# Optimization experiments

Hardware: AMD Instinct MI355X
Metric: run time of the kernel (lower is better)

Reference implementation:

```python
import jax, jax.numpy as jnp
import numpy as np

N_NODES = 50000
N_EDGES = 800000
IN_FEATS = 64
K = 4
OUT_FEATS = 256


def setup_inputs() -> dict:
    key = jax.random.key(0)
    k1, k2, k3, k4, k5 = jax.random.split(key, 5)
    signal = jax.random.normal(k1, (N_NODES, IN_FEATS), dtype=jnp.float32)
    src = jax.random.randint(k2, (N_EDGES,), 0, N_NODES, dtype=jnp.int32)
    dst = jax.random.randint(k3, (N_EDGES,), 0, N_NODES, dtype=jnp.int32)
    lambda_max = jnp.array([2.0], dtype=jnp.float32)  # normalized Laplacian bound
    W = jax.random.normal(k4, (IN_FEATS * K, OUT_FEATS), dtype=jnp.float32) * (1.0 / np.sqrt(IN_FEATS * K))
    b = jax.random.normal(k5, (OUT_FEATS,), dtype=jnp.float32) * 0.01
    return {"signal": signal, "src": src, "dst": dst, "lambda_max": lambda_max, "W": W, "b": b}


def reference(signal, src, dst, lambda_max, W, b):
    n = signal.shape[0]
    # in-degrees, clamped to >= 1, then D^{-1/2}
    deg = jax.ops.segment_sum(jnp.ones_like(dst, dtype=signal.dtype), dst, num_segments=n)
    d_sqrt = jnp.power(jnp.clip(deg, 1.0), -0.5)[:, None]  # [N,1]

    def unn_laplacian(x):
        # D^{-1/2} A D^{-1/2} x via gather-from-src, scatter-sum-to-dst
        h = (x * d_sqrt)[src]                                   # [E,f]
        agg = jax.ops.segment_sum(h, dst, num_segments=n)       # [N,f]
        return agg * d_sqrt

    X0 = signal
    Xs = [X0]
    if K > 1:
        re_norm = 2.0 / lambda_max  # broadcasts over nodes ([1] -> [N,f])
        X1 = -re_norm * unn_laplacian(X0) + X0 * (re_norm - 1.0)
        Xs.append(X1)
        for _ in range(2, K):
            Xi = -2.0 * re_norm * unn_laplacian(X1) + X1 * 2.0 * (re_norm - 1.0) - X0
            Xs.append(Xi)
            X1, X0 = Xi, X1
    Xt = jnp.concatenate(Xs, axis=1)  # [N, f*K]
    return jax.nn.relu(Xt @ W + b)
```

## Files before the change

kernel.cpp:

```cpp
#include <hip/hip_runtime.h>

#define NN 50000
#define NE 800000
#define F  64
#define FK 256
#define OUTF 256
#define CAP 48
#define NT 3128

#define NPART 8
#define PART_NODES 6250
#define FILL_CHUNKS 256
#define CHUNK_E 3125

typedef __attribute__((ext_vector_type(8))) short s16x8;
typedef __attribute__((ext_vector_type(4))) float f32x4;

static __device__ __forceinline__ unsigned short f2bf(float f) {
    unsigned u = __float_as_uint(f);
    u += 0x7fffu + ((u >> 16) & 1u);
    return (unsigned short)(u >> 16);
}
static __device__ __forceinline__ float bf2f(int h) {
    return __uint_as_float(((unsigned)(h & 0xffff)) << 16);
}

__global__ __launch_bounds__(256) void fill_kernel(const int* __restrict__ src,
                                                   const int* __restrict__ dst,
                                                   int* __restrict__ cnt,
                                                   int* __restrict__ csr) {
    int part  = blockIdx.x & (NPART - 1);
    int chunk = blockIdx.x >> 3;
    int lo = part * PART_NODES;
    int e0 = chunk * CHUNK_E;
    int e1 = e0 + CHUNK_E;
    for (int e = e0 + threadIdx.x; e < e1; e += 256) {
        int d = dst[e];
        int s = src[e];
        if ((unsigned)(d - lo) < (unsigned)PART_NODES) {
            int k = atomicAdd(&cnt[d], 1);
            if (k < CAP) csr[d * CAP + k] = s;
        }
    }
}

__global__ void dsqrt_kernel(const int* __restrict__ cnt, float* __restrict__ dsq) {
    int n = blockIdx.x * blockDim.x + threadIdx.x;
    if (n < NN) dsq[n] = rsqrtf(fmaxf((float)cnt[n], 1.0f));
}


__global__ void copy0_kernel(const float* __restrict__ sig,
                             unsigned short* __restrict__ XrowH,
                             unsigned short* __restrict__ XrowL,
                             unsigned short* __restrict__ XfH) {
    int i = blockIdx.x * blockDim.x + threadIdx.x;
    if (i >= NN * 16) return;
    int n = i >> 4, fq = i & 15;
    float4 v = *(const float4*)&sig[n * F + fq * 4];
    unsigned short h0 = f2bf(v.x), h1 = f2bf(v.y), h2 = f2bf(v.z), h3 = f2bf(v.w);
    unsigned short l0 = f2bf(v.x - bf2f(h0)), l1 = f2bf(v.y - bf2f(h1));
    unsigned short l2 = f2bf(v.z - bf2f(h2)), l3 = f2bf(v.w - bf2f(h3));
    *(ushort4*)&XrowH[(size_t)n * 192 + fq * 4] = make_ushort4(h0, h1, h2, h3);
    *(ushort4*)&XrowL[(size_t)n * 192 + fq * 4] = make_ushort4(l0, l1, l2, l3);
    int t = n >> 4, m = n & 15;
    int k0 = fq >> 3, qq = (fq >> 1) & 3, half = fq & 1;
    size_t base = ((size_t)((t * 8 + k0) * 64 + qq * 16 + m)) * 8 + half * 4;
    *(ushort4*)&XfH[base] = make_ushort4(h0, h1, h2, h3);
}

__global__ void convw_kernel(const float* __restrict__ W,
                             unsigned short* __restrict__ WfH,
                             unsigned short* __restrict__ WfL) {
    int id = blockIdx.x * blockDim.x + threadIdx.x;
    if (id >= 8192) return;
    int lane = id & 63, k0 = (id >> 6) & 7, ct = id >> 9;
    int n = lane & 15, q = lane >> 4;
    s16x8 h, l;
    #pragma unroll
    for (int j = 0; j < 8; ++j) {
        float x = W[(k0 * 32 + q * 8 + j) * OUTF + ct * 16 + n];
        unsigned short hh = f2bf(x);
        h[j] = (short)hh;
        l[j] = (short)f2bf(x - bf2f(hh));
    }
    ((s16x8*)WfH)[id] = h;
    ((s16x8*)WfL)[id] = l;
}

__global__ __launch_bounds__(256) void lap_kernel(const int* __restrict__ cnt,
                                                  const int* __restrict__ csr,
                                                  const float* __restrict__ dsq,
                                                  const float* __restrict__ lm,
                                                  unsigned short* __restrict__ XrowH,
                                                  unsigned short* __restrict__ XrowL,
                                                  unsigned short* __restrict__ XfH, int p) {
    int wid  = (blockIdx.x * blockDim.x + threadIdx.x) >> 6;
    int lane = threadIdx.x & 63;
    int q  = lane >> 4;
    int fq = lane & 15;
    if (wid >= NN) return;
    int n  = wid;
    int dg = min(cnt[n], CAP);
    int cin = p - 1;
    int foff = fq << 2;

    float ax = 0.f, ay = 0.f, az = 0.f, aw = 0.f;
    for (int k = q; k < dg; k += 16) {
        int s0 = csr[n * CAP + k];
        int s1 = (k + 4  < dg) ? csr[n * CAP + k + 4]  : s0;
        int s2 = (k + 8  < dg) ? csr[n * CAP + k + 8]  : s0;
        int s3 = (k + 12 < dg) ? csr[n * CAP + k + 12] : s0;
        float d0 = dsq[s0];
        float d1 = (k + 4  < dg) ? dsq[s1] : 0.f;
        float d2 = (k + 8  < dg) ? dsq[s2] : 0.f;
        float d3 = (k + 12 < dg) ? dsq[s3] : 0.f;
        ushort4 h0 = *(const ushort4*)&XrowH[((size_t)s0 * 3 + cin) * 64 + foff];
        ushort4 h1 = *(const ushort4*)&XrowH[((size_t)s1 * 3 + cin) * 64 + foff];
        ushort4 h2 = *(const ushort4*)&XrowH[((size_t)s2 * 3 + cin) * 64 + foff];
        ushort4 h3 = *(const ushort4*)&XrowH[((size_t)s3 * 3 + cin) * 64 + foff];
        ax += bf2f(h0.x) * d0 + bf2f(h1.x) * d1 + bf2f(h2.x) * d2 + bf2f(h3.x) * d3;
        ay += bf2f(h0.y) * d0 + bf2f(h1.y) * d1 + bf2f(h2.y) * d2 + bf2f(h3.y) * d3;
        az += bf2f(h0.z) * d0 + bf2f(h1.z) * d1 + bf2f(h2.z) * d2 + bf2f(h3.z) * d3;
        aw += bf2f(h0.w) * d0 + bf2f(h1.w) * d1 + bf2f(h2.w) * d2 + bf2f(h3.w) * d3;
    }
    ax += __shfl_xor(ax, 16); ax += __shfl_xor(ax, 32);
    ay += __shfl_xor(ay, 16); ay += __shfl_xor(ay, 32);
    az += __shfl_xor(az, 16); az += __shfl_xor(az, 32);
    aw += __shfl_xor(aw, 16); aw += __shfl_xor(aw, 32);

    float rn = 2.0f / lm[0];
    float dn = dsq[n];
    ushort4 xh = *(const ushort4*)&XrowH[((size_t)n * 3 + cin) * 64 + foff];
    ushort4 xl = *(const ushort4*)&XrowL[((size_t)n * 3 + cin) * 64 + foff];
    float x1x = bf2f(xh.x) + bf2f(xl.x);
    float x1y = bf2f(xh.y) + bf2f(xl.y);
    float x1z = bf2f(xh.z) + bf2f(xl.z);
    float x1w = bf2f(xh.w) + bf2f(xl.w);
    float rx, ry, rz, rw;
    if (p == 1) {
        float c1 = rn - 1.0f;
        rx = -rn * dn * ax + x1x * c1;
        ry = -rn * dn * ay + x1y * c1;
        rz = -rn * dn * az + x1z * c1;
        rw = -rn * dn * aw + x1w * c1;
    } else {
        ushort4 zh = *(const ushort4*)&XrowH[((size_t)n * 3 + (p - 2)) * 64 + foff];
        ushort4 zl = *(const ushort4*)&XrowL[((size_t)n * 3 + (p - 2)) * 64 + foff];
        float c1 = 2.0f * (rn - 1.0f);
        rx = -2.0f * rn * dn * ax + x1x * c1 - (bf2f(zh.x) + bf2f(zl.x));
        ry = -2.0f * rn * dn * ay + x1y * c1 - (bf2f(zh.y) + bf2f(zl.y));
        rz = -2.0f * rn * dn * az + x1z * c1 - (bf2f(zh.z) + bf2f(zl.z));
        rw = -2.0f * rn * dn * aw + x1w * c1 - (bf2f(zh.w) + bf2f(zl.w));
    }
    unsigned short h0 = f2bf(rx), h1 = f2bf(ry), h2 = f2bf(rz), h3 = f2bf(rw);

    if (q == 0 && p < 3) {
        *(ushort4*)&XrowH[((size_t)n * 3 + p) * 64 + foff] = make_ushort4(h0, h1, h2, h3);
    } else if (q == 2 && p < 3) {
        unsigned short l0 = f2bf(rx - bf2f(h0)), l1 = f2bf(ry - bf2f(h1));
        unsigned short l2 = f2bf(rz - bf2f(h2)), l3 = f2bf(rw - bf2f(h3));
        *(ushort4*)&XrowL[((size_t)n * 3 + p) * 64 + foff] = make_ushort4(l0, l1, l2, l3);
    } else if (q == 1) {
        int t = n >> 4, m = n & 15;
        int k0 = p * 2 + (fq >> 3), qq = (fq >> 1) & 3, half = fq & 1;
        size_t fbase = ((size_t)((t * 8 + k0) * 64 + qq * 16 + m)) * 8 + half * 4;
        *(ushort4*)&XfH[fbase] = make_ushort4(h0, h1, h2, h3);
    }
}

__global__ __launch_bounds__(512, 2) void gemm_kernel(const unsigned short* __restrict__ XfH,
                                                      const unsigned short* __restrict__ WfH,
                                                      const unsigned short* __restrict__ WfL,
                                                      const float* __restrict__ b,
                                                      float* __restrict__ out) {
    int lane = threadIdx.x & 63;
    int w    = threadIdx.x >> 6;
    int rh = w & 1, cg = w >> 1;
    int m = lane & 15, q = lane >> 4;
    int bt0 = blockIdx.x * 8;
    const s16x8* AH = (const s16x8*)XfH;
    const s16x8* BH = (const s16x8*)WfH;
    const s16x8* BL = (const s16x8*)WfL;

    f32x4 acc[4][4];
    #pragma unroll
    for (int rt = 0; rt < 4; ++rt)
        #pragma unroll
        for (int c = 0; c < 4; ++c) acc[rt][c] = (f32x4){0.f, 0.f, 0.f, 0.f};

    #pragma unroll
    for (int k0 = 0; k0 < 8; ++k0) {
        s16x8 a[4];
        #pragma unroll
        for (int rt = 0; rt < 4; ++rt)
            a[rt] = AH[((bt0 + rh * 4 + rt) * 8 + k0) * 64 + lane];
        #pragma unroll
        for (int c = 0; c < 4; ++c) {
            int ct = cg * 4 + c;
            s16x8 bh = BH[(ct * 8 + k0) * 64 + lane];
            s16x8 bl = BL[(ct * 8 + k0) * 64 + lane];
            #pragma unroll
            for (int rt = 0; rt < 4; ++rt) {
                acc[rt][c] = __builtin_amdgcn_mfma_f32_16x16x32_bf16(a[rt], bh, acc[rt][c], 0, 0, 0);
                acc[rt][c] = __builtin_amdgcn_mfma_f32_16x16x32_bf16(a[rt], bl, acc[rt][c], 0, 0, 0);
            }
        }
    }

    #pragma unroll
    for (int rt = 0; rt < 4; ++rt) {
        int rbase = (bt0 + rh * 4 + rt) * 16 + q * 4;
        #pragma unroll
        for (int c = 0; c < 4; ++c) {
            int col = (cg * 4 + c) * 16 + m;
            float bv = b[col];
            #pragma unroll
            for (int i = 0; i < 4; ++i) {
                int r = rbase + i;
                if (r < NN) out[r * OUTF + col] = fmaxf(acc[rt][c][i] + bv, 0.0f);
            }
        }
    }
}

extern "C" void kernel_launch(void* const* d_in, const int* in_sizes, int n_in,
                              void* d_out, int out_size, void* d_ws, size_t ws_size,
                              hipStream_t stream) {
    const float* signal     = (const float*)d_in[0];
    const int*   src        = (const int*)  d_in[1];
    const int*   dst        = (const int*)  d_in[2];
    const float* lambda_max = (const float*)d_in[3];
    const float* W          = (const float*)d_in[4];
    const float* b          = (const float*)d_in[5];
    float* out = (float*)d_out;

    int*   cnt = (int*)d_ws;
    int*   csr = cnt + NN;
    float* dsq = (float*)(csr + NN * CAP);
    unsigned short* XrowH = (unsigned short*)(dsq + NN);
    unsigned short* XrowL = XrowH + (size_t)NN * 192;
    unsigned short* XfH   = XrowL + (size_t)NN * 192;
    unsigned short* WfH   = XfH + (size_t)NT * 4096;
    unsigned short* WfL   = WfH + 65536;

    hipMemsetAsync(cnt, 0, NN * sizeof(int), stream);
    fill_kernel<<<NPART * FILL_CHUNKS, 256, 0, stream>>>(src, dst, cnt, csr);
    dsqrt_kernel<<<(NN + 255) / 256, 256, 0, stream>>>(cnt, dsq);
    copy0_kernel<<<(NN * 16 + 255) / 256, 256, 0, stream>>>(signal, XrowH, XrowL, XfH);
    convw_kernel<<<32, 256, 0, stream>>>(W, WfH, WfL);

    for (int p = 1; p <= 3; ++p)
        lap_kernel<<<NN / 4, 256, 0, stream>>>(cnt, csr, dsq, lambda_max, XrowH, XrowL, XfH, p);

    gemm_kernel<<<391, 512, 0, stream>>>(XfH, WfH, WfL, b, out);
}
```

Baseline: 245.2 us.

## Store pre-scaled rows, pack two nodes per wave, halve GEMM row tile

The gather buffers now hold X scaled by D^{-1/2}, so the Laplacian inner loop no longer does a per-neighbour dsq lookup. The true X is recovered from the stored values with a sqrt(degree) factor. Each wave now processes two nodes with 8 independent gathers in flight per lane, and the src load in the CSR fill is deferred until the partition check passes. The GEMM tile is halved to 2 row tiles per wave with twice as many blocks. This trades extra rescaling arithmetic and some rounding drift from the pre-scaled bf16 storage for less dependent gather latency and more parallelism.

```diff
diff --git a/kernel.cpp b/kernel.cpp
--- a/kernel.cpp
+++ b/kernel.cpp
@@ -36,8 +36,8 @@
     int e1 = e0 + CHUNK_E;
     for (int e = e0 + threadIdx.x; e < e1; e += 256) {
         int d = dst[e];
-        int s = src[e];
         if ((unsigned)(d - lo) < (unsigned)PART_NODES) {
+            int s = src[e];
             int k = atomicAdd(&cnt[d], 1);
             if (k < CAP) csr[d * CAP + k] = s;
         }
@@ -51,22 +51,26 @@
 
 
 __global__ void copy0_kernel(const float* __restrict__ sig,
+                             const float* __restrict__ dsq,
                              unsigned short* __restrict__ XrowH,
                              unsigned short* __restrict__ XrowL,
                              unsigned short* __restrict__ XfH) {
     int i = blockIdx.x * blockDim.x + threadIdx.x;
     if (i >= NN * 16) return;
     int n = i >> 4, fq = i & 15;
+    float d = dsq[n];
     float4 v = *(const float4*)&sig[n * F + fq * 4];
-    unsigned short h0 = f2bf(v.x), h1 = f2bf(v.y), h2 = f2bf(v.z), h3 = f2bf(v.w);
-    unsigned short l0 = f2bf(v.x - bf2f(h0)), l1 = f2bf(v.y - bf2f(h1));
-    unsigned short l2 = f2bf(v.z - bf2f(h2)), l3 = f2bf(v.w - bf2f(h3));
+    float yx = v.x * d, yy = v.y * d, yz = v.z * d, yw = v.w * d;
+    unsigned short h0 = f2bf(yx), h1 = f2bf(yy), h2 = f2bf(yz), h3 = f2bf(yw);
+    unsigned short l0 = f2bf(yx - bf2f(h0)), l1 = f2bf(yy - bf2f(h1));
+    unsigned short l2 = f2bf(yz - bf2f(h2)), l3 = f2bf(yw - bf2f(h3));
     *(ushort4*)&XrowH[(size_t)n * 192 + fq * 4] = make_ushort4(h0, h1, h2, h3);
     *(ushort4*)&XrowL[(size_t)n * 192 + fq * 4] = make_ushort4(l0, l1, l2, l3);
+    unsigned short u0 = f2bf(v.x), u1 = f2bf(v.y), u2 = f2bf(v.z), u3 = f2bf(v.w);
     int t = n >> 4, m = n & 15;
     int k0 = fq >> 3, qq = (fq >> 1) & 3, half = fq & 1;
     size_t base = ((size_t)((t * 8 + k0) * 64 + qq * 16 + m)) * 8 + half * 4;
-    *(ushort4*)&XfH[base] = make_ushort4(h0, h1, h2, h3);
+    *(ushort4*)&XfH[base] = make_ushort4(u0, u1, u2, u3);
 }
 
 __global__ void convw_kernel(const float* __restrict__ W,
@@ -95,48 +99,57 @@
                                                   unsigned short* __restrict__ XrowH,
                                                   unsigned short* __restrict__ XrowL,
                                                   unsigned short* __restrict__ XfH, int p) {
+    int lane = threadIdx.x & 63;
+    int half = lane >> 5;
+    int sub  = lane & 31;
+    int q2   = sub >> 4;
+    int fq   = sub & 15;
     int wid  = (blockIdx.x * blockDim.x + threadIdx.x) >> 6;
-    int lane = threadIdx.x & 63;
-    int q  = lane >> 4;
-    int fq = lane & 15;
-    if (wid >= NN) return;
-    int n  = wid;
-    int dg = min(cnt[n], CAP);
+    int n    = wid * 2 + half;
+    if (n >= NN) return;
+    int dgf = cnt[n];
+    int dg  = min(dgf, CAP);
     int cin = p - 1;
     int foff = fq << 2;
 
     float ax = 0.f, ay = 0.f, az = 0.f, aw = 0.f;
-    for (int k = q; k < dg; k += 16) {
-        int s0 = csr[n * CAP + k];
-        int s1 = (k + 4  < dg) ? csr[n * CAP + k + 4]  : s0;
-        int s2 = (k + 8  < dg) ? csr[n * CAP + k + 8]  : s0;
-        int s3 = (k + 12 < dg) ? csr[n * CAP + k + 12] : s0;
-        float d0 = dsq[s0];
-        float d1 = (k + 4  < dg) ? dsq[s1] : 0.f;
-        float d2 = (k + 8  < dg) ? dsq[s2] : 0.f;
-        float d3 = (k + 12 < dg) ? dsq[s3] : 0.f;
-        ushort4 h0 = *(const ushort4*)&XrowH[((size_t)s0 * 3 + cin) * 64 + foff];
-        ushort4 h1 = *(const ushort4*)&XrowH[((size_t)s1 * 3 + cin) * 64 + foff];
-        ushort4 h2 = *(const ushort4*)&XrowH[((size_t)s2 * 3 + cin) * 64 + foff];
-        ushort4 h3 = *(const ushort4*)&XrowH[((size_t)s3 * 3 + cin) * 64 + foff];
-        ax += bf2f(h0.x) * d0 + bf2f(h1.x) * d1 + bf2f(h2.x) * d2 + bf2f(h3.x) * d3;
-        ay += bf2f(h0.y) * d0 + bf2f(h1.y) * d1 + bf2f(h2.y) * d2 + bf2f(h3.y) * d3;
-        az += bf2f(h0.z) * d0 + bf2f(h1.z) * d1 + bf2f(h2.z) * d2 + bf2f(h3.z) * d3;
-        aw += bf2f(h0.w) * d0 + bf2f(h1.w) * d1 + bf2f(h2.w) * d2 + bf2f(h3.w) * d3;
-    }
-    ax += __shfl_xor(ax, 16); ax += __shfl_xor(ax, 32);
-    ay += __shfl_xor(ay, 16); ay += __shfl_xor(ay, 32);
-    az += __shfl_xor(az, 16); az += __shfl_xor(az, 32);
-    aw += __shfl_xor(aw, 16); aw += __shfl_xor(aw, 32);
+    for (int k = 0; k < dg; k += 16) {
+        int   s[8];
+        float w[8];
+        ushort4 h[8];
+        #pragma unroll
+        for (int j = 0; j < 8; ++j) {
+            int slot = k + q2 + 2 * j;
+            int ok   = slot < dg;
+            int si   = csr[n * CAP + slot];
+            s[j] = ok ? si : 0;
+            w[j] = ok ? 1.0f : 0.0f;
+        }
+        #pragma unroll
+        for (int j = 0; j < 8; ++j)
+            h[j] = *(const ushort4*)&XrowH[((size_t)s[j] * 3 + cin) * 64 + foff];
+        #pragma unroll
+        for (int j = 0; j < 8; ++j) {
+            ax += bf2f(h[j].x) * w[j];
+            ay += bf2f(h[j].y) * w[j];
+            az += bf2f(h[j].z) * w[j];
+            aw += bf2f(h[j].w) * w[j];
+        }
+    }
+    ax += __shfl_xor(ax, 16);
+    ay += __shfl_xor(ay, 16);
+    az += __shfl_xor(az, 16);
+    aw += __shfl_xor(aw, 16);
 
     float rn = 2.0f / lm[0];
     float dn = dsq[n];
+    float sq = sqrtf(fmaxf((float)dgf, 1.0f));
     ushort4 xh = *(const ushort4*)&XrowH[((size_t)n * 3 + cin) * 64 + foff];
     ushort4 xl = *(const ushort4*)&XrowL[((size_t)n * 3 + cin) * 64 + foff];
-    float x1x = bf2f(xh.x) + bf2f(xl.x);
-    float x1y = bf2f(xh.y) + bf2f(xl.y);
-    float x1z = bf2f(xh.z) + bf2f(xl.z);
-    float x1w = bf2f(xh.w) + bf2f(xl.w);
+    float x1x = (bf2f(xh.x) + bf2f(xl.x)) * sq;
+    float x1y = (bf2f(xh.y) + bf2f(xl.y)) * sq;
+    float x1z = (bf2f(xh.z) + bf2f(xl.z)) * sq;
+    float x1w = (bf2f(xh.w) + bf2f(xl.w)) * sq;
     float rx, ry, rz, rw;
     if (p == 1) {
         float c1 = rn - 1.0f;
@@ -148,24 +161,26 @@
         ushort4 zh = *(const ushort4*)&XrowH[((size_t)n * 3 + (p - 2)) * 64 + foff];
         ushort4 zl = *(const ushort4*)&XrowL[((size_t)n * 3 + (p - 2)) * 64 + foff];
         float c1 = 2.0f * (rn - 1.0f);
-        rx = -2.0f * rn * dn * ax + x1x * c1 - (bf2f(zh.x) + bf2f(zl.x));
-        ry = -2.0f * rn * dn * ay + x1y * c1 - (bf2f(zh.y) + bf2f(zl.y));
-        rz = -2.0f * rn * dn * az + x1z * c1 - (bf2f(zh.z) + bf2f(zl.z));
-        rw = -2.0f * rn * dn * aw + x1w * c1 - (bf2f(zh.w) + bf2f(zl.w));
-    }
-    unsigned short h0 = f2bf(rx), h1 = f2bf(ry), h2 = f2bf(rz), h3 = f2bf(rw);
-
-    if (q == 0 && p < 3) {
-        *(ushort4*)&XrowH[((size_t)n * 3 + p) * 64 + foff] = make_ushort4(h0, h1, h2, h3);
-    } else if (q == 2 && p < 3) {
-        unsigned short l0 = f2bf(rx - bf2f(h0)), l1 = f2bf(ry - bf2f(h1));
-        unsigned short l2 = f2bf(rz - bf2f(h2)), l3 = f2bf(rw - bf2f(h3));
+        rx = -2.0f * rn * dn * ax + x1x * c1 - (bf2f(zh.x) + bf2f(zl.x)) * sq;
+        ry = -2.0f * rn * dn * ay + x1y * c1 - (bf2f(zh.y) + bf2f(zl.y)) * sq;
+        rz = -2.0f * rn * dn * az + x1z * c1 - (bf2f(zh.z) + bf2f(zl.z)) * sq;
+        rw = -2.0f * rn * dn * aw + x1w * c1 - (bf2f(zh.w) + bf2f(zl.w)) * sq;
+    }
+
+    float yx = rx * dn, yy = ry * dn, yz = rz * dn, yw = rw * dn;
+    unsigned short yh0 = f2bf(yx), yh1 = f2bf(yy), yh2 = f2bf(yz), yh3 = f2bf(yw);
+    if (q2 == 0) {
+        if (p < 3)
+            *(ushort4*)&XrowH[((size_t)n * 3 + p) * 64 + foff] = make_ushort4(yh0, yh1, yh2, yh3);
+        unsigned short u0 = f2bf(rx), u1 = f2bf(ry), u2 = f2bf(rz), u3 = f2bf(rw);
+        int t = n >> 4, m = n & 15;
+        int k0 = p * 2 + (fq >> 3), qq = (fq >> 1) & 3, hf = fq & 1;
+        size_t fbase = ((size_t)((t * 8 + k0) * 64 + qq * 16 + m)) * 8 + hf * 4;
+        *(ushort4*)&XfH[fbase] = make_ushort4(u0, u1, u2, u3);
+    } else if (p < 3) {
+        unsigned short l0 = f2bf(yx - bf2f(yh0)), l1 = f2bf(yy - bf2f(yh1));
+        unsigned short l2 = f2bf(yz - bf2f(yh2)), l3 = f2bf(yw - bf2f(yh3));
         *(ushort4*)&XrowL[((size_t)n * 3 + p) * 64 + foff] = make_ushort4(l0, l1, l2, l3);
-    } else if (q == 1) {
-        int t = n >> 4, m = n & 15;
-        int k0 = p * 2 + (fq >> 3), qq = (fq >> 1) & 3, half = fq & 1;
-        size_t fbase = ((size_t)((t * 8 + k0) * 64 + qq * 16 + m)) * 8 + half * 4;
-        *(ushort4*)&XfH[fbase] = make_ushort4(h0, h1, h2, h3);
     }
 }
 
@@ -178,30 +193,30 @@
     int w    = threadIdx.x >> 6;
     int rh = w & 1, cg = w >> 1;
     int m = lane & 15, q = lane >> 4;
-    int bt0 = blockIdx.x * 8;
+    int bt0 = blockIdx.x * 4;
     const s16x8* AH = (const s16x8*)XfH;
     const s16x8* BH = (const s16x8*)WfH;
     const s16x8* BL = (const s16x8*)WfL;
 
-    f32x4 acc[4][4];
-    #pragma unroll
-    for (int rt = 0; rt < 4; ++rt)
+    f32x4 acc[2][4];
+    #pragma unroll
+    for (int rt = 0; rt < 2; ++rt)
         #pragma unroll
         for (int c = 0; c < 4; ++c) acc[rt][c] = (f32x4){0.f, 0.f, 0.f, 0.f};
 
     #pragma unroll
     for (int k0 = 0; k0 < 8; ++k0) {
-        s16x8 a[4];
-        #pragma unroll
-        for (int rt = 0; rt < 4; ++rt)
-            a[rt] = AH[((bt0 + rh * 4 + rt) * 8 + k0) * 64 + lane];
+        s16x8 a[2];
+        #pragma unroll
+        for (int rt = 0; rt < 2; ++rt)
+            a[rt] = AH[((bt0 + rh * 2 + rt) * 8 + k0) * 64 + lane];
         #pragma unroll
         for (int c = 0; c < 4; ++c) {
             int ct = cg * 4 + c;
             s16x8 bh = BH[(ct * 8 + k0) * 64 + lane];
             s16x8 bl = BL[(ct * 8 + k0) * 64 + lane];
             #pragma unroll
-            for (int rt = 0; rt < 4; ++rt) {
+            for (int rt = 0; rt < 2; ++rt) {
                 acc[rt][c] = __builtin_amdgcn_mfma_f32_16x16x32_bf16(a[rt], bh, acc[rt][c], 0, 0, 0);
                 acc[rt][c] = __builtin_amdgcn_mfma_f32_16x16x32_bf16(a[rt], bl, acc[rt][c], 0, 0, 0);
             }
@@ -209,8 +224,8 @@
     }
 
     #pragma unroll
-    for (int rt = 0; rt < 4; ++rt) {
-        int rbase = (bt0 + rh * 4 + rt) * 16 + q * 4;
+    for (int rt = 0; rt < 2; ++rt) {
+        int rbase = (bt0 + rh * 2 + rt) * 16 + q * 4;
         #pragma unroll
         for (int c = 0; c < 4; ++c) {
             int col = (cg * 4 + c) * 16 + m;
@@ -247,11 +262,11 @@
     hipMemsetAsync(cnt, 0, NN * sizeof(int), stream);
     fill_kernel<<<NPART * FILL_CHUNKS, 256, 0, stream>>>(src, dst, cnt, csr);
     dsqrt_kernel<<<(NN + 255) / 256, 256, 0, stream>>>(cnt, dsq);
-    copy0_kernel<<<(NN * 16 + 255) / 256, 256, 0, stream>>>(signal, XrowH, XrowL, XfH);
+    copy0_kernel<<<(NN * 16 + 255) / 256, 256, 0, stream>>>(signal, dsq, XrowH, XrowL, XfH);
     convw_kernel<<<32, 256, 0, stream>>>(W, WfH, WfL);
 
     for (int p = 1; p <= 3; ++p)
-        lap_kernel<<<NN / 4, 256, 0, stream>>>(cnt, csr, dsq, lambda_max, XrowH, XrowL, XfH, p);
-
-    gemm_kernel<<<391, 512, 0, stream>>>(XfH, WfH, WfL, b, out);
-}
+        lap_kernel<<<NN / 8, 256, 0, stream>>>(cnt, csr, dsq, lambda_max, XrowH, XrowL, XfH, p);
+
+    gemm_kernel<<<782, 512, 0, stream>>>(XfH, WfH, WfL, b, out);
+}
```

New measurement: 232.7 us. -5.1%, faster.
